# Kernel tuning notes

Measured on AMD Instinct MI355X. Metric: run time of the kernel, lower is better.

## Reference

```python
import jax, jax.numpy as jnp
import numpy as np

EPS = 1e-5
NEG_SLOPE = 0.01  # F.leaky_relu default

N0, N1, N2 = 100000, 25000, 5000
E0, E1 = 800000, 160000
D_IN, D_HID, D_OUT = 256, 256, 128


def setup_inputs() -> dict:
    key = jax.random.key(0)
    ks = jax.random.split(key, 16)
    inp = {
        "x": jax.random.normal(ks[0], (N0, D_IN), dtype=jnp.float32),
        "src0": jax.random.randint(ks[1], (E0,), 0, N0, dtype=jnp.int32),
        "dst0": jax.random.randint(ks[2], (E0,), 0, N1, dtype=jnp.int32),
        "val0": jnp.arange(E0, dtype=jnp.int32),
        "src1": jax.random.randint(ks[3], (E1,), 0, N1, dtype=jnp.int32),
        "dst1": jax.random.randint(ks[4], (E1,), 0, N2, dtype=jnp.int32),
        "val1": jnp.arange(E1, dtype=jnp.int32),
        "timestamps": jax.random.randint(ks[5], (E0 + E1,), 0, 100, dtype=jnp.int32),
        "time": 50,
        "interval": 10,
        # SAGEConv layer 1 (in -> hidden): lin_l (bias) on aggregated, lin_r (no bias) on root
        "W1l": jax.random.normal(ks[6], (D_IN, D_HID), dtype=jnp.float32) / np.sqrt(D_IN),
        "W1r": jax.random.normal(ks[7], (D_IN, D_HID), dtype=jnp.float32) / np.sqrt(D_IN),
        "b1": jnp.zeros((D_HID,), dtype=jnp.float32),
        # BatchNorm1d params (eval mode: running stats)
        "g1": jnp.ones((D_HID,), dtype=jnp.float32),
        "bt1": jnp.zeros((D_HID,), dtype=jnp.float32),
        "rm1": jax.random.normal(ks[8], (D_HID,), dtype=jnp.float32) * 0.1,
        "rv1": jax.random.uniform(ks[9], (D_HID,), dtype=jnp.float32) + 0.5,
        # SAGEConv layer 2 (hidden -> out)
        "W2l": jax.random.normal(ks[10], (D_HID, D_OUT), dtype=jnp.float32) / np.sqrt(D_HID),
        "W2r": jax.random.normal(ks[11], (D_HID, D_OUT), dtype=jnp.float32) / np.sqrt(D_HID),
        "b2": jnp.zeros((D_OUT,), dtype=jnp.float32),
    }
    return inp


def _time_mask(val, timestamps, time, interval):
    # time_sparse keeps edges whose timestamp is in {time, ..., time+interval-1}
    ts = timestamps[val]
    return (ts >= time) & (ts < time + interval)


def _sage_conv(x_src, x_tgt, src, dst, mask, Wl, Wr, b, n_tgt):
    m = mask.astype(x_src.dtype)
    msg = x_src[src] * m[:, None]               # [E, D] gather + mask
    agg = jax.ops.segment_sum(msg, dst, num_segments=n_tgt)
    deg = jax.ops.segment_sum(m, dst, num_segments=n_tgt)
    agg = agg / jnp.maximum(deg, 1.0)[:, None]  # mean aggregation
    return agg @ Wl + b + x_tgt @ Wr


def reference(x, src0, dst0, val0, src1, dst1, val1, timestamps, time, interval,
              W1l, W1r, b1, g1, bt1, rm1, rv1, W2l, W2r, b2):
    # layer 0: N0 -> N1
    mask0 = _time_mask(val0, timestamps, time, interval)
    h = _sage_conv(x, x[:N1], src0, dst0, mask0, W1l, W1r, b1, N1)
    # BatchNorm1d (eval) + leaky_relu; dropout is identity in eval
    h = (h - rm1) * jax.lax.rsqrt(rv1 + EPS) * g1 + bt1
    h = jnp.where(h >= 0, h, NEG_SLOPE * h)
    # layer 1: N1 -> N2
    mask1 = _time_mask(val1, timestamps, time, interval)
    out = _sage_conv(h, h[:N2], src1, dst1, mask1, W2l, W2r, b2, N2)
    return out, mask1
```

## Files before the change

kernel.cpp:

```cpp
#include <hip/hip_runtime.h>

#define N1c 25000
#define N2c 5000
#define Dc 256
#define DOUTc 128
#define EPSc 1e-5f
#define NEGc 0.01f
#define CAPc 32

typedef __attribute__((ext_vector_type(8))) short short8;
typedef __attribute__((ext_vector_type(4))) float f32x4;

__device__ __forceinline__ ushort f2bf(float f) {
    unsigned u = __float_as_uint(f);
    u += 0x7fffu + ((u >> 16) & 1u);
    return (ushort)(u >> 16);
}
__device__ __forceinline__ float bf2f(ushort u) {
    return __uint_as_float(((unsigned)u) << 16);
}

__global__ __launch_bounds__(256) void prep_fill(
    const int* __restrict__ src0, const int* __restrict__ dst0, const int* __restrict__ val0,
    const int* __restrict__ src1, const int* __restrict__ dst1, const int* __restrict__ val1,
    const int* __restrict__ ts, const int* __restrict__ time_p, const int* __restrict__ itv_p,
    const float* __restrict__ W1l, const float* __restrict__ W1r,
    const float* __restrict__ W2l, const float* __restrict__ W2r,
    int E0, int E1,
    ushort* __restrict__ Bt1, ushort* __restrict__ Bt2,
    int* __restrict__ cnt0, int* __restrict__ cnt1,
    int* __restrict__ eidx0, int* __restrict__ eidx1,
    float* __restrict__ mask_out) {
    const int flat = blockIdx.x * blockDim.x + threadIdx.x;
    const int NT = gridDim.x * blockDim.x;
    const int t0 = *time_p, iv = *itv_p;

    for (int i = flat; i < 256 * 512; i += NT) {
        int n = i >> 9, k = i & 511;
        float v = (k < 256) ? W1l[(size_t)k * 256 + n] : W1r[(size_t)(k - 256) * 256 + n];
        Bt1[i] = f2bf(v);
    }
    for (int i = flat; i < 128 * 512; i += NT) {
        int n = i >> 9, k = i & 511;
        float v = (k < 256) ? W2l[(size_t)k * 128 + n] : W2r[(size_t)(k - 256) * 128 + n];
        Bt2[i] = f2bf(v);
    }
    for (int e = flat; e < E0; e += NT) {
        int t = ts[val0[e]];
        if (t >= t0 && t < t0 + iv) {
            int d = dst0[e];
            int pos = atomicAdd(&cnt0[d], 1);
            if (pos < CAPc) eidx0[d * CAPc + pos] = src0[e];
        }
    }
    for (int e = flat; e < E1; e += NT) {
        int t = ts[val1[e]];
        bool m = (t >= t0 && t < t0 + iv);
        mask_out[e] = m ? 1.0f : 0.0f;
        if (m) {
            int d = dst1[e];
            int pos = atomicAdd(&cnt1[d], 1);
            if (pos < CAPc) eidx1[d * CAPc + pos] = src1[e];
        }
    }
}

template <int VARIANT, int BMT, int NJW>
__global__ __launch_bounds__(512) void fused_gemm(
    const void* __restrict__ Asrc,
    const int* __restrict__ cnt, const int* __restrict__ eidx,
    const int* __restrict__ src, const int* __restrict__ dst,
    const int* __restrict__ val, const int* __restrict__ ts,
    const int* __restrict__ time_p, const int* __restrict__ itv_p, int E,
    const ushort* __restrict__ Bt,
    const float* __restrict__ bias,
    const float* __restrict__ g, const float* __restrict__ bt,
    const float* __restrict__ rm, const float* __restrict__ rv,
    void* __restrict__ Cout, int M) {
    constexpr int RT = BMT / 16;
    constexpr int RPW = BMT / 8;
    __shared__ ushort As[BMT][536];
    const int tid = threadIdx.x;
    const int wave = tid >> 6, lane = tid & 63;
    const int quad = lane >> 4, l16 = lane & 15;
    const int m0 = blockIdx.x * BMT;
    const float* Xf = (const float*)Asrc;
    const ushort* Hb = (const ushort*)Asrc;

    for (int i = 0; i < RPW; ++i) {
        int r = wave * RPW + i;
        int m = m0 + r;
        if (m >= M) {
            *(ushort4*)&As[r][lane * 4] = make_ushort4(0, 0, 0, 0);
            *(ushort4*)&As[r][256 + lane * 4] = make_ushort4(0, 0, 0, 0);
            continue;
        }
        int c = cnt[m];
        int my = (lane < CAPc) ? eidx[m * CAPc + lane] : 0;
        float4 a0 = make_float4(0.f, 0.f, 0.f, 0.f);
        float4 a1 = make_float4(0.f, 0.f, 0.f, 0.f);
        if (c <= CAPc) {
            int j = 0;
            for (; j + 1 < c; j += 2) {
                int s0 = __shfl(my, j, 64);
                int s1 = __shfl(my, j + 1, 64);
                if (VARIANT == 0) {
                    float4 v0 = *(const float4*)(Xf + (size_t)s0 * Dc + lane * 4);
                    float4 v1 = *(const float4*)(Xf + (size_t)s1 * Dc + lane * 4);
                    a0.x += v0.x; a0.y += v0.y; a0.z += v0.z; a0.w += v0.w;
                    a1.x += v1.x; a1.y += v1.y; a1.z += v1.z; a1.w += v1.w;
                } else {
                    ushort4 v0 = *(const ushort4*)(Hb + (size_t)s0 * Dc + lane * 4);
                    ushort4 v1 = *(const ushort4*)(Hb + (size_t)s1 * Dc + lane * 4);
                    a0.x += bf2f(v0.x); a0.y += bf2f(v0.y); a0.z += bf2f(v0.z); a0.w += bf2f(v0.w);
                    a1.x += bf2f(v1.x); a1.y += bf2f(v1.y); a1.z += bf2f(v1.z); a1.w += bf2f(v1.w);
                }
            }
            if (j < c) {
                int s0 = __shfl(my, j, 64);
                if (VARIANT == 0) {
                    float4 v0 = *(const float4*)(Xf + (size_t)s0 * Dc + lane * 4);
                    a0.x += v0.x; a0.y += v0.y; a0.z += v0.z; a0.w += v0.w;
                } else {
                    ushort4 v0 = *(const ushort4*)(Hb + (size_t)s0 * Dc + lane * 4);
                    a0.x += bf2f(v0.x); a0.y += bf2f(v0.y); a0.z += bf2f(v0.z); a0.w += bf2f(v0.w);
                }
            }
        } else {
            int t0 = *time_p, iv = *itv_p;
            for (int e = 0; e < E; ++e) {
                if (dst[e] != m) continue;
                int t = ts[val[e]];
                if (t >= t0 && t < t0 + iv) {
                    if (VARIANT == 0) {
                        float4 v = *(const float4*)(Xf + (size_t)src[e] * Dc + lane * 4);
                        a0.x += v.x; a0.y += v.y; a0.z += v.z; a0.w += v.w;
                    } else {
                        ushort4 v = *(const ushort4*)(Hb + (size_t)src[e] * Dc + lane * 4);
                        a0.x += bf2f(v.x); a0.y += bf2f(v.y); a0.z += bf2f(v.z); a0.w += bf2f(v.w);
                    }
                }
            }
        }
        a0.x += a1.x; a0.y += a1.y; a0.z += a1.z; a0.w += a1.w;
        float inv = 1.0f / fmaxf((float)c, 1.0f);
        ushort4 o;
        o.x = f2bf(a0.x * inv); o.y = f2bf(a0.y * inv);
        o.z = f2bf(a0.z * inv); o.w = f2bf(a0.w * inv);
        *(ushort4*)&As[r][lane * 4] = o;
        if (VARIANT == 0) {
            float4 rt = *(const float4*)(Xf + (size_t)m * Dc + lane * 4);
            ushort4 ro;
            ro.x = f2bf(rt.x); ro.y = f2bf(rt.y); ro.z = f2bf(rt.z); ro.w = f2bf(rt.w);
            *(ushort4*)&As[r][256 + lane * 4] = ro;
        } else {
            *(ushort4*)&As[r][256 + lane * 4] = *(const ushort4*)(Hb + (size_t)m * Dc + lane * 4);
        }
    }
    __syncthreads();

    f32x4 acc[RT][NJW] = {};
    const ushort* Bw = Bt + (size_t)((wave * NJW) * 16 + l16) * 512 + quad * 8;
    for (int k0 = 0; k0 < 512; k0 += 32) {
        short8 af[RT];
#pragma unroll
        for (int rt = 0; rt < RT; ++rt)
            af[rt] = *(const short8*)&As[rt * 16 + l16][k0 + quad * 8];
        uint4 bfr[NJW];
#pragma unroll
        for (int jj = 0; jj < NJW; ++jj)
            bfr[jj] = *(const uint4*)(Bw + (size_t)jj * 16 * 512 + k0);
#pragma unroll
        for (int jj = 0; jj < NJW; ++jj) {
            short8 bf = *reinterpret_cast<const short8*>(&bfr[jj]);
#pragma unroll
            for (int rt = 0; rt < RT; ++rt)
                acc[rt][jj] = __builtin_amdgcn_mfma_f32_16x16x32_bf16(af[rt], bf, acc[rt][jj], 0, 0, 0);
        }
    }

#pragma unroll
    for (int jj = 0; jj < NJW; ++jj) {
        int gn = (wave * NJW + jj) * 16 + l16;
        float sc = 1.f, sh = bias[gn];
        if (VARIANT == 0) {
            float s = g[gn] * rsqrtf(rv[gn] + EPSc);
            sh = (bias[gn] - rm[gn]) * s + bt[gn];
            sc = s;
        }
#pragma unroll
        for (int rt = 0; rt < RT; ++rt) {
            int gmb = m0 + rt * 16 + quad * 4;
#pragma unroll
            for (int rr = 0; rr < 4; ++rr) {
                int gm = gmb + rr;
                if (gm >= M) continue;
                float v = acc[rt][jj][rr];
                if (VARIANT == 0) {
                    v = v * sc + sh;
                    v = v >= 0.f ? v : NEGc * v;
                    ((ushort*)Cout)[(size_t)gm * Dc + gn] = f2bf(v);
                } else {
                    ((float*)Cout)[(size_t)gm * DOUTc + gn] = v + sh;
                }
            }
        }
    }
}

extern "C" void kernel_launch(void* const* d_in, const int* in_sizes, int n_in,
                              void* d_out, int out_size, void* d_ws, size_t ws_size,
                              hipStream_t stream) {
    const float* x    = (const float*)d_in[0];
    const int* src0   = (const int*)d_in[1];
    const int* dst0   = (const int*)d_in[2];
    const int* val0   = (const int*)d_in[3];
    const int* src1   = (const int*)d_in[4];
    const int* dst1   = (const int*)d_in[5];
    const int* val1   = (const int*)d_in[6];
    const int* ts     = (const int*)d_in[7];
    const int* time_p = (const int*)d_in[8];
    const int* itv_p  = (const int*)d_in[9];
    const float* W1l  = (const float*)d_in[10];
    const float* W1r  = (const float*)d_in[11];
    const float* b1   = (const float*)d_in[12];
    const float* g1   = (const float*)d_in[13];
    const float* bt1  = (const float*)d_in[14];
    const float* rm1  = (const float*)d_in[15];
    const float* rv1  = (const float*)d_in[16];
    const float* W2l  = (const float*)d_in[17];
    const float* W2r  = (const float*)d_in[18];
    const float* b2   = (const float*)d_in[19];
    int E0 = in_sizes[1];
    int E1 = in_sizes[4];
    float* out = (float*)d_out;

    ushort* h    = (ushort*)d_ws;
    ushort* Bt1  = h    + (size_t)N1c * Dc;
    ushort* Bt2  = Bt1  + 256 * 512;
    int* ip      = (int*)(Bt2 + 128 * 512);
    int* cnt0    = ip;             ip += N1c;
    int* cnt1    = ip;             ip += N2c;
    int* eidx0   = ip;             ip += N1c * CAPc;
    int* eidx1   = ip;             ip += N2c * CAPc;
    float* mask_tail = out + (size_t)N2c * DOUTc;

    hipMemsetAsync(cnt0, 0, (size_t)(N1c + N2c) * sizeof(int), stream);

    prep_fill<<<2048, 256, 0, stream>>>(
        src0, dst0, val0, src1, dst1, val1, ts, time_p, itv_p,
        W1l, W1r, W2l, W2r, E0, E1, Bt1, Bt2,
        cnt0, cnt1, eidx0, eidx1, mask_tail);
    fused_gemm<0, 32, 2><<<(N1c + 31) / 32, 512, 0, stream>>>(
        x, cnt0, eidx0, src0, dst0, val0, ts, time_p, itv_p, E0,
        Bt1, b1, g1, bt1, rm1, rv1, h, N1c);
    fused_gemm<1, 16, 1><<<(N2c + 15) / 16, 512, 0, stream>>>(
        h, cnt1, eidx1, src1, dst1, val1, ts, time_p, itv_p, E1,
        Bt2, b2, nullptr, nullptr, nullptr, nullptr, out, N2c);
}
```

Before: 248.7 us.

## Batch gather loads across rows to raise memory-level parallelism in aggregation

```diff
diff --git a/kernel.cpp b/kernel.cpp
--- a/kernel.cpp
+++ b/kernel.cpp
@@ -19,6 +19,8 @@
 __device__ __forceinline__ float bf2f(ushort u) {
     return __uint_as_float(((unsigned)u) << 16);
 }
+__device__ __forceinline__ int imin(int a, int b) { return a < b ? a : b; }
+__device__ __forceinline__ int imax(int a, int b) { return a > b ? a : b; }
 
 __global__ __launch_bounds__(256) void prep_fill(
     const int* __restrict__ src0, const int* __restrict__ dst0, const int* __restrict__ val0,
@@ -87,74 +89,124 @@
     const float* Xf = (const float*)Asrc;
     const ushort* Hb = (const ushort*)Asrc;
 
+    int ms_[RPW], cs_[RPW], my_[RPW];
+#pragma unroll
     for (int i = 0; i < RPW; ++i) {
-        int r = wave * RPW + i;
-        int m = m0 + r;
-        if (m >= M) {
-            *(ushort4*)&As[r][lane * 4] = make_ushort4(0, 0, 0, 0);
-            *(ushort4*)&As[r][256 + lane * 4] = make_ushort4(0, 0, 0, 0);
-            continue;
-        }
-        int c = cnt[m];
-        int my = (lane < CAPc) ? eidx[m * CAPc + lane] : 0;
-        float4 a0 = make_float4(0.f, 0.f, 0.f, 0.f);
-        float4 a1 = make_float4(0.f, 0.f, 0.f, 0.f);
-        if (c <= CAPc) {
-            int j = 0;
-            for (; j + 1 < c; j += 2) {
-                int s0 = __shfl(my, j, 64);
-                int s1 = __shfl(my, j + 1, 64);
-                if (VARIANT == 0) {
-                    float4 v0 = *(const float4*)(Xf + (size_t)s0 * Dc + lane * 4);
-                    float4 v1 = *(const float4*)(Xf + (size_t)s1 * Dc + lane * 4);
-                    a0.x += v0.x; a0.y += v0.y; a0.z += v0.z; a0.w += v0.w;
-                    a1.x += v1.x; a1.y += v1.y; a1.z += v1.z; a1.w += v1.w;
-                } else {
-                    ushort4 v0 = *(const ushort4*)(Hb + (size_t)s0 * Dc + lane * 4);
-                    ushort4 v1 = *(const ushort4*)(Hb + (size_t)s1 * Dc + lane * 4);
-                    a0.x += bf2f(v0.x); a0.y += bf2f(v0.y); a0.z += bf2f(v0.z); a0.w += bf2f(v0.w);
-                    a1.x += bf2f(v1.x); a1.y += bf2f(v1.y); a1.z += bf2f(v1.z); a1.w += bf2f(v1.w);
+        ms_[i] = m0 + wave * RPW + i;
+        cs_[i] = (ms_[i] < M) ? cnt[ms_[i]] : 0;
+    }
+#pragma unroll
+    for (int i = 0; i < RPW; ++i)
+        my_[i] = (ms_[i] < M && lane < CAPc) ? eidx[ms_[i] * CAPc + lane] : 0;
+    float4 rtf_[RPW];
+    ushort4 rtb_[RPW];
+#pragma unroll
+    for (int i = 0; i < RPW; ++i) {
+        int mm = imax(0, imin(ms_[i], M - 1));
+        if (VARIANT == 0) rtf_[i] = *(const float4*)(Xf + (size_t)mm * Dc + lane * 4);
+        else              rtb_[i] = *(const ushort4*)(Hb + (size_t)mm * Dc + lane * 4);
+    }
+#pragma unroll
+    for (int i = 0; i < RPW; ++i)
+        my_[i] = (lane < cs_[i]) ? my_[i] : 0;
+
+    float4 acc_[RPW];
+#pragma unroll
+    for (int i = 0; i < RPW; ++i) acc_[i] = make_float4(0.f, 0.f, 0.f, 0.f);
+
+#pragma unroll
+    for (int p = 0; p < RPW; p += 2) {
+        float4 vf[2][4];
+        ushort4 vb[2][4];
+        int ccs[2];
+#pragma unroll
+        for (int q = 0; q < 2; ++q) {
+            int cc = imin(cs_[p + q], CAPc);
+            ccs[q] = cc;
+#pragma unroll
+            for (int u = 0; u < 4; ++u) {
+                int e = imax(0, imin(u, cc - 1));
+                int s = __shfl(my_[p + q], e, 64);
+                if (VARIANT == 0) vf[q][u] = *(const float4*)(Xf + (size_t)s * Dc + lane * 4);
+                else              vb[q][u] = *(const ushort4*)(Hb + (size_t)s * Dc + lane * 4);
+            }
+        }
+#pragma unroll
+        for (int q = 0; q < 2; ++q) {
+            int i = p + q;
+            int cc = ccs[q];
+#pragma unroll
+            for (int u = 0; u < 4; ++u) {
+                if (u < cc) {
+                    if (VARIANT == 0) {
+                        acc_[i].x += vf[q][u].x; acc_[i].y += vf[q][u].y;
+                        acc_[i].z += vf[q][u].z; acc_[i].w += vf[q][u].w;
+                    } else {
+                        acc_[i].x += bf2f(vb[q][u].x); acc_[i].y += bf2f(vb[q][u].y);
+                        acc_[i].z += bf2f(vb[q][u].z); acc_[i].w += bf2f(vb[q][u].w);
+                    }
                 }
             }
-            if (j < c) {
-                int s0 = __shfl(my, j, 64);
-                if (VARIANT == 0) {
-                    float4 v0 = *(const float4*)(Xf + (size_t)s0 * Dc + lane * 4);
-                    a0.x += v0.x; a0.y += v0.y; a0.z += v0.z; a0.w += v0.w;
-                } else {
-                    ushort4 v0 = *(const ushort4*)(Hb + (size_t)s0 * Dc + lane * 4);
-                    a0.x += bf2f(v0.x); a0.y += bf2f(v0.y); a0.z += bf2f(v0.z); a0.w += bf2f(v0.w);
+            for (int jb = 4; jb < cc; jb += 4) {
+#pragma unroll
+                for (int u = 0; u < 4; ++u) {
+                    int e = imin(jb + u, cc - 1);
+                    int s = __shfl(my_[i], e, 64);
+                    if (jb + u < cc) {
+                        if (VARIANT == 0) {
+                            float4 v = *(const float4*)(Xf + (size_t)s * Dc + lane * 4);
+                            acc_[i].x += v.x; acc_[i].y += v.y; acc_[i].z += v.z; acc_[i].w += v.w;
+                        } else {
+                            ushort4 v = *(const ushort4*)(Hb + (size_t)s * Dc + lane * 4);
+                            acc_[i].x += bf2f(v.x); acc_[i].y += bf2f(v.y);
+                            acc_[i].z += bf2f(v.z); acc_[i].w += bf2f(v.w);
+                        }
+                    }
                 }
             }
-        } else {
+        }
+    }
+#pragma unroll
+    for (int i = 0; i < RPW; ++i) {
+        if (cs_[i] > CAPc) {
+            float4 a = make_float4(0.f, 0.f, 0.f, 0.f);
             int t0 = *time_p, iv = *itv_p;
             for (int e = 0; e < E; ++e) {
-                if (dst[e] != m) continue;
+                if (dst[e] != ms_[i]) continue;
                 int t = ts[val[e]];
                 if (t >= t0 && t < t0 + iv) {
                     if (VARIANT == 0) {
                         float4 v = *(const float4*)(Xf + (size_t)src[e] * Dc + lane * 4);
-                        a0.x += v.x; a0.y += v.y; a0.z += v.z; a0.w += v.w;
+                        a.x += v.x; a.y += v.y; a.z += v.z; a.w += v.w;
                     } else {
                         ushort4 v = *(const ushort4*)(Hb + (size_t)src[e] * Dc + lane * 4);
-                        a0.x += bf2f(v.x); a0.y += bf2f(v.y); a0.z += bf2f(v.z); a0.w += bf2f(v.w);
+                        a.x += bf2f(v.x); a.y += bf2f(v.y); a.z += bf2f(v.z); a.w += bf2f(v.w);
                     }
                 }
             }
-        }
-        a0.x += a1.x; a0.y += a1.y; a0.z += a1.z; a0.w += a1.w;
-        float inv = 1.0f / fmaxf((float)c, 1.0f);
+            acc_[i] = a;
+        }
+    }
+#pragma unroll
+    for (int i = 0; i < RPW; ++i) {
+        int r = wave * RPW + i;
+        if (ms_[i] >= M) {
+            *(ushort4*)&As[r][lane * 4] = make_ushort4(0, 0, 0, 0);
+            *(ushort4*)&As[r][256 + lane * 4] = make_ushort4(0, 0, 0, 0);
+            continue;
+        }
+        float inv = 1.0f / fmaxf((float)cs_[i], 1.0f);
         ushort4 o;
-        o.x = f2bf(a0.x * inv); o.y = f2bf(a0.y * inv);
-        o.z = f2bf(a0.z * inv); o.w = f2bf(a0.w * inv);
+        o.x = f2bf(acc_[i].x * inv); o.y = f2bf(acc_[i].y * inv);
+        o.z = f2bf(acc_[i].z * inv); o.w = f2bf(acc_[i].w * inv);
         *(ushort4*)&As[r][lane * 4] = o;
         if (VARIANT == 0) {
-            float4 rt = *(const float4*)(Xf + (size_t)m * Dc + lane * 4);
             ushort4 ro;
-            ro.x = f2bf(rt.x); ro.y = f2bf(rt.y); ro.z = f2bf(rt.z); ro.w = f2bf(rt.w);
+            ro.x = f2bf(rtf_[i].x); ro.y = f2bf(rtf_[i].y);
+            ro.z = f2bf(rtf_[i].z); ro.w = f2bf(rtf_[i].w);
             *(ushort4*)&As[r][256 + lane * 4] = ro;
         } else {
-            *(ushort4*)&As[r][256 + lane * 4] = *(const ushort4*)(Hb + (size_t)m * Dc + lane * 4);
+            *(ushort4*)&As[r][256 + lane * 4] = rtb_[i];
         }
     }
     __syncthreads();
```

After: 248.9 us. No clear change (+0.1%).

## Fuse whole pipeline into one cooperative persistent kernel with grid syncs

Applied to the files above, without the earlier changes.

```diff
diff --git a/kernel.cpp b/kernel.cpp
--- a/kernel.cpp
+++ b/kernel.cpp
@@ -1,4 +1,7 @@
 #include <hip/hip_runtime.h>
+#include <hip/hip_cooperative_groups.h>
+
+namespace cg = cooperative_groups;
 
 #define N1c 25000
 #define N2c 5000
@@ -18,6 +21,250 @@
 }
 __device__ __forceinline__ float bf2f(ushort u) {
     return __uint_as_float(((unsigned)u) << 16);
+}
+__device__ __forceinline__ unsigned pack2(float lo, float hi) {
+    return ((unsigned)f2bf(lo)) | (((unsigned)f2bf(hi)) << 16);
+}
+
+struct MegaParams {
+    const float* x;
+    const int *src0, *dst0, *val0, *src1, *dst1, *val1, *ts, *time_p, *itv_p;
+    const float *W1l, *W1r, *b1, *g1, *bt1, *rm1, *rv1, *W2l, *W2r, *b2;
+    int E0, E1;
+    ushort *agg0, *h, *agg1, *Bt1, *Bt2;
+    int *cnt0, *cnt1, *eidx0, *eidx1;
+    float *mask_out, *out;
+};
+
+template <int SRC>
+__device__ __forceinline__ void gather_phase(
+    const void* Xsrc, const int* cnt, const int* eidx,
+    const int* src, const int* dst, const int* val, const int* ts,
+    int t0, int iv, int E, ushort* agg, int n, int gw, int nw, int lane) {
+    const float* Xf = (const float*)Xsrc;
+    const ushort* Hb = (const ushort*)Xsrc;
+    for (int row = gw; row < n; row += nw) {
+        int c = cnt[row];
+        int my = (lane < CAPc) ? eidx[row * CAPc + lane] : 0;
+        my = (lane < c) ? my : 0;
+        float4 a = make_float4(0.f, 0.f, 0.f, 0.f);
+        float4 a2 = make_float4(0.f, 0.f, 0.f, 0.f);
+        if (c <= CAPc) {
+            int j = 0;
+            for (; j + 1 < c; j += 2) {
+                int s0 = __shfl(my, j, 64);
+                int s1 = __shfl(my, j + 1, 64);
+                if (SRC == 0) {
+                    float4 v0 = *(const float4*)(Xf + (size_t)s0 * Dc + lane * 4);
+                    float4 v1 = *(const float4*)(Xf + (size_t)s1 * Dc + lane * 4);
+                    a.x += v0.x; a.y += v0.y; a.z += v0.z; a.w += v0.w;
+                    a2.x += v1.x; a2.y += v1.y; a2.z += v1.z; a2.w += v1.w;
+                } else {
+                    ushort4 v0 = *(const ushort4*)(Hb + (size_t)s0 * Dc + lane * 4);
+                    ushort4 v1 = *(const ushort4*)(Hb + (size_t)s1 * Dc + lane * 4);
+                    a.x += bf2f(v0.x); a.y += bf2f(v0.y);
+                    a.z += bf2f(v0.z); a.w += bf2f(v0.w);
+                    a2.x += bf2f(v1.x); a2.y += bf2f(v1.y);
+                    a2.z += bf2f(v1.z); a2.w += bf2f(v1.w);
+                }
+            }
+            if (j < c) {
+                int s0 = __shfl(my, j, 64);
+                if (SRC == 0) {
+                    float4 v0 = *(const float4*)(Xf + (size_t)s0 * Dc + lane * 4);
+                    a.x += v0.x; a.y += v0.y; a.z += v0.z; a.w += v0.w;
+                } else {
+                    ushort4 v0 = *(const ushort4*)(Hb + (size_t)s0 * Dc + lane * 4);
+                    a.x += bf2f(v0.x); a.y += bf2f(v0.y);
+                    a.z += bf2f(v0.z); a.w += bf2f(v0.w);
+                }
+            }
+        } else {
+            for (int e = 0; e < E; ++e) {
+                if (dst[e] != row) continue;
+                int t = ts[val[e]];
+                if (t >= t0 && t < t0 + iv) {
+                    if (SRC == 0) {
+                        float4 v = *(const float4*)(Xf + (size_t)src[e] * Dc + lane * 4);
+                        a.x += v.x; a.y += v.y; a.z += v.z; a.w += v.w;
+                    } else {
+                        ushort4 v = *(const ushort4*)(Hb + (size_t)src[e] * Dc + lane * 4);
+                        a.x += bf2f(v.x); a.y += bf2f(v.y);
+                        a.z += bf2f(v.z); a.w += bf2f(v.w);
+                    }
+                }
+            }
+        }
+        a.x += a2.x; a.y += a2.y; a.z += a2.z; a.w += a2.w;
+        float inv = 1.0f / fmaxf((float)c, 1.0f);
+        ushort4 o;
+        o.x = f2bf(a.x * inv); o.y = f2bf(a.y * inv);
+        o.z = f2bf(a.z * inv); o.w = f2bf(a.w * inv);
+        *(ushort4*)(agg + (size_t)row * Dc + lane * 4) = o;
+    }
+}
+
+template <int VARIANT>
+__device__ __forceinline__ void gemm_tile(
+    ushort (*As)[536], int mt,
+    const ushort* Alo, const void* A2, const ushort* Bt,
+    const float* bias, const float* g, const float* bt,
+    const float* rm, const float* rv, void* Cout, int M, int tid) {
+    constexpr int NJW = (VARIANT == 0) ? 4 : 2;
+    const int wave = tid >> 6, lane = tid & 63;
+    const int quad = lane >> 4, l16 = lane & 15;
+    const int m0 = mt * 32;
+#pragma unroll
+    for (int i = 0; i < 8; ++i) {
+        int r = wave * 8 + i, m = m0 + r;
+        if (m < M) {
+            *(ushort4*)&As[r][lane * 4] =
+                *(const ushort4*)(Alo + (size_t)m * Dc + lane * 4);
+            if (VARIANT == 0) {
+                float4 xf = *(const float4*)((const float*)A2 + (size_t)m * Dc + lane * 4);
+                ushort4 ro;
+                ro.x = f2bf(xf.x); ro.y = f2bf(xf.y);
+                ro.z = f2bf(xf.z); ro.w = f2bf(xf.w);
+                *(ushort4*)&As[r][256 + lane * 4] = ro;
+            } else {
+                *(ushort4*)&As[r][256 + lane * 4] =
+                    *(const ushort4*)((const ushort*)A2 + (size_t)m * Dc + lane * 4);
+            }
+        } else {
+            *(ushort4*)&As[r][lane * 4] = make_ushort4(0, 0, 0, 0);
+            *(ushort4*)&As[r][256 + lane * 4] = make_ushort4(0, 0, 0, 0);
+        }
+    }
+    __syncthreads();
+    f32x4 acc[2][NJW] = {};
+    const ushort* Bw = Bt + (size_t)((wave * NJW) * 16 + l16) * 512 + quad * 8;
+    for (int k0 = 0; k0 < 512; k0 += 32) {
+        short8 af[2];
+        af[0] = *(const short8*)&As[l16][k0 + quad * 8];
+        af[1] = *(const short8*)&As[16 + l16][k0 + quad * 8];
+        uint4 bfr[NJW];
+#pragma unroll
+        for (int jj = 0; jj < NJW; ++jj)
+            bfr[jj] = *(const uint4*)(Bw + (size_t)jj * 16 * 512 + k0);
+#pragma unroll
+        for (int jj = 0; jj < NJW; ++jj) {
+            short8 bf = *reinterpret_cast<const short8*>(&bfr[jj]);
+#pragma unroll
+            for (int rt = 0; rt < 2; ++rt)
+                acc[rt][jj] = __builtin_amdgcn_mfma_f32_16x16x32_bf16(af[rt], bf, acc[rt][jj], 0, 0, 0);
+        }
+    }
+    __syncthreads();
+#pragma unroll
+    for (int jj = 0; jj < NJW; ++jj) {
+        int gn = (wave * NJW + jj) * 16 + l16;
+        float sc = 1.f, sh = bias[gn];
+        if (VARIANT == 0) {
+            float s = g[gn] * rsqrtf(rv[gn] + EPSc);
+            sh = (bias[gn] - rm[gn]) * s + bt[gn];
+            sc = s;
+        }
+#pragma unroll
+        for (int rt = 0; rt < 2; ++rt) {
+            int gmb = m0 + rt * 16 + quad * 4;
+#pragma unroll
+            for (int rr = 0; rr < 4; ++rr) {
+                int gm = gmb + rr;
+                if (gm >= M) continue;
+                float v = acc[rt][jj][rr];
+                if (VARIANT == 0) {
+                    v = v * sc + sh;
+                    v = v >= 0.f ? v : NEGc * v;
+                    ((ushort*)Cout)[(size_t)gm * Dc + gn] = f2bf(v);
+                } else {
+                    ((float*)Cout)[(size_t)gm * DOUTc + gn] = v + sh;
+                }
+            }
+        }
+    }
+}
+
+__global__ __launch_bounds__(256, 4) void mega(MegaParams P) {
+    cg::grid_group grid = cg::this_grid();
+    __shared__ ushort As[32][536];
+    const int tid = threadIdx.x, bid = blockIdx.x, nb = gridDim.x;
+    const int flat = bid * 256 + tid, NT = nb * 256;
+    const int lane = tid & 63;
+    const int gw = flat >> 6, nw = NT >> 6;
+    const int t0 = *P.time_p, iv = *P.itv_p;
+
+    for (int i = flat; i < N1c + N2c; i += NT) {
+        if (i < N1c) P.cnt0[i] = 0; else P.cnt1[i - N1c] = 0;
+    }
+    {
+        float (*tl)[33] = (float (*)[33])As;
+        const int tx = tid & 31, ty = tid >> 5;
+        for (int t = bid; t < 192; t += nb) {
+            const bool L1 = t < 128;
+            const int tt = L1 ? t : t - 128;
+            const int ntn = L1 ? 8 : 4;
+            const int kt = tt / ntn, nt = tt % ntn;
+            const int k0 = kt * 32, n0 = nt * 32;
+            const float* Wl = L1 ? P.W1l : P.W2l;
+            const float* Wr = L1 ? P.W1r : P.W2r;
+            const int nst = L1 ? 256 : 128;
+            ushort* Bt = L1 ? P.Bt1 : P.Bt2;
+#pragma unroll
+            for (int rr = 0; rr < 4; ++rr) {
+                int r = ty * 4 + rr;
+                int k = k0 + r;
+                tl[r][tx] = (k < 256) ? Wl[(size_t)k * nst + n0 + tx]
+                                      : Wr[(size_t)(k - 256) * nst + n0 + tx];
+            }
+            __syncthreads();
+#pragma unroll
+            for (int rr = 0; rr < 4; ++rr) {
+                int r = ty * 4 + rr;
+                Bt[(size_t)(n0 + r) * 512 + k0 + tx] = f2bf(tl[tx][r]);
+            }
+            __syncthreads();
+        }
+    }
+    for (int e = flat; e < P.E1; e += NT) {
+        int t = P.ts[P.val1[e]];
+        P.mask_out[e] = (t >= t0 && t < t0 + iv) ? 1.0f : 0.0f;
+    }
+    grid.sync();
+
+    for (int e = flat; e < P.E0; e += NT) {
+        int t = P.ts[P.val0[e]];
+        if (t >= t0 && t < t0 + iv) {
+            int d = P.dst0[e];
+            int pos = atomicAdd(&P.cnt0[d], 1);
+            if (pos < CAPc) P.eidx0[d * CAPc + pos] = P.src0[e];
+        }
+    }
+    for (int e = flat; e < P.E1; e += NT) {
+        int t = P.ts[P.val1[e]];
+        if (t >= t0 && t < t0 + iv) {
+            int d = P.dst1[e];
+            int pos = atomicAdd(&P.cnt1[d], 1);
+            if (pos < CAPc) P.eidx1[d * CAPc + pos] = P.src1[e];
+        }
+    }
+    grid.sync();
+
+    gather_phase<0>(P.x, P.cnt0, P.eidx0, P.src0, P.dst0, P.val0, P.ts,
+                    t0, iv, P.E0, P.agg0, N1c, gw, nw, lane);
+    grid.sync();
+
+    for (int mt = bid; mt * 32 < N1c; mt += nb)
+        gemm_tile<0>(As, mt, P.agg0, P.x, P.Bt1, P.b1, P.g1, P.bt1, P.rm1, P.rv1,
+                     P.h, N1c, tid);
+    grid.sync();
+
+    gather_phase<1>(P.h, P.cnt1, P.eidx1, P.src1, P.dst1, P.val1, P.ts,
+                    t0, iv, P.E1, P.agg1, N2c, gw, nw, lane);
+    grid.sync();
+
+    for (int mt = bid; mt * 32 < N2c; mt += nb)
+        gemm_tile<1>(As, mt, P.agg1, P.h, P.Bt2, P.b2, nullptr, nullptr, nullptr,
+                     nullptr, P.out, N2c, tid);
 }
 
 __global__ __launch_bounds__(256) void prep_fill(
@@ -34,16 +281,32 @@
     const int flat = blockIdx.x * blockDim.x + threadIdx.x;
     const int NT = gridDim.x * blockDim.x;
     const int t0 = *time_p, iv = *itv_p;
-
-    for (int i = flat; i < 256 * 512; i += NT) {
-        int n = i >> 9, k = i & 511;
-        float v = (k < 256) ? W1l[(size_t)k * 256 + n] : W1r[(size_t)(k - 256) * 256 + n];
-        Bt1[i] = f2bf(v);
-    }
-    for (int i = flat; i < 128 * 512; i += NT) {
-        int n = i >> 9, k = i & 511;
-        float v = (k < 256) ? W2l[(size_t)k * 128 + n] : W2r[(size_t)(k - 256) * 128 + n];
-        Bt2[i] = f2bf(v);
+    __shared__ float tl[32][33];
+    const int tx = threadIdx.x & 31, ty = threadIdx.x >> 5;
+    for (int t = blockIdx.x; t < 192; t += gridDim.x) {
+        const bool L1 = t < 128;
+        const int tt = L1 ? t : t - 128;
+        const int ntn = L1 ? 8 : 4;
+        const int kt = tt / ntn, nt = tt % ntn;
+        const int k0 = kt * 32, n0 = nt * 32;
+        const float* Wl = L1 ? W1l : W2l;
+        const float* Wr = L1 ? W1r : W2r;
+        const int nst = L1 ? 256 : 128;
+        ushort* Bt = L1 ? Bt1 : Bt2;
+#pragma unroll
+        for (int rr = 0; rr < 4; ++rr) {
+            int r = ty * 4 + rr;
+            int k = k0 + r;
+            tl[r][tx] = (k < 256) ? Wl[(size_t)k * nst + n0 + tx]
+                                  : Wr[(size_t)(k - 256) * nst + n0 + tx];
+        }
+        __syncthreads();
+#pragma unroll
+        for (int rr = 0; rr < 4; ++rr) {
+            int r = ty * 4 + rr;
+            Bt[(size_t)(n0 + r) * 512 + k0 + tx] = f2bf(tl[tx][r]);
+        }
+        __syncthreads();
     }
     for (int e = flat; e < E0; e += NT) {
         int t = ts[val0[e]];
@@ -65,147 +328,30 @@
     }
 }
 
-template <int VARIANT, int BMT, int NJW>
-__global__ __launch_bounds__(512) void fused_gemm(
-    const void* __restrict__ Asrc,
-    const int* __restrict__ cnt, const int* __restrict__ eidx,
-    const int* __restrict__ src, const int* __restrict__ dst,
-    const int* __restrict__ val, const int* __restrict__ ts,
-    const int* __restrict__ time_p, const int* __restrict__ itv_p, int E,
-    const ushort* __restrict__ Bt,
-    const float* __restrict__ bias,
+template <int SRC>
+__global__ void gather_k(const void* X, const int* __restrict__ cnt,
+                         const int* __restrict__ eidx,
+                         const int* __restrict__ src, const int* __restrict__ dst,
+                         const int* __restrict__ val, const int* __restrict__ ts,
+                         const int* __restrict__ time_p, const int* __restrict__ itv_p,
+                         int E, ushort* __restrict__ agg, int n) {
+    int wave = (blockIdx.x * blockDim.x + threadIdx.x) >> 6;
+    int lane = threadIdx.x & 63;
+    if (wave >= n) return;
+    gather_phase<SRC>(X, cnt, eidx, src, dst, val, ts, *time_p, *itv_p, E,
+                      agg, n, wave, 1 << 30, lane);
+}
+
+template <int VARIANT>
+__global__ __launch_bounds__(256) void gemm_k(
+    const ushort* __restrict__ Alo, const void* __restrict__ A2,
+    const ushort* __restrict__ Bt, const float* __restrict__ bias,
     const float* __restrict__ g, const float* __restrict__ bt,
     const float* __restrict__ rm, const float* __restrict__ rv,
     void* __restrict__ Cout, int M) {
-    constexpr int RT = BMT / 16;
-    constexpr int RPW = BMT / 8;
-    __shared__ ushort As[BMT][536];
-    const int tid = threadIdx.x;
-    const int wave = tid >> 6, lane = tid & 63;
-    const int quad = lane >> 4, l16 = lane & 15;
-    const int m0 = blockIdx.x * BMT;
-    const float* Xf = (const float*)Asrc;
-    const ushort* Hb = (const ushort*)Asrc;
-
-    for (int i = 0; i < RPW; ++i) {
-        int r = wave * RPW + i;
-        int m = m0 + r;
-        if (m >= M) {
-            *(ushort4*)&As[r][lane * 4] = make_ushort4(0, 0, 0, 0);
-            *(ushort4*)&As[r][256 + lane * 4] = make_ushort4(0, 0, 0, 0);
-            continue;
-        }
-        int c = cnt[m];
-        int my = (lane < CAPc) ? eidx[m * CAPc + lane] : 0;
-        float4 a0 = make_float4(0.f, 0.f, 0.f, 0.f);
-        float4 a1 = make_float4(0.f, 0.f, 0.f, 0.f);
-        if (c <= CAPc) {
-            int j = 0;
-            for (; j + 1 < c; j += 2) {
-                int s0 = __shfl(my, j, 64);
-                int s1 = __shfl(my, j + 1, 64);
-                if (VARIANT == 0) {
-                    float4 v0 = *(const float4*)(Xf + (size_t)s0 * Dc + lane * 4);
-                    float4 v1 = *(const float4*)(Xf + (size_t)s1 * Dc + lane * 4);
-                    a0.x += v0.x; a0.y += v0.y; a0.z += v0.z; a0.w += v0.w;
-                    a1.x += v1.x; a1.y += v1.y; a1.z += v1.z; a1.w += v1.w;
-                } else {
-                    ushort4 v0 = *(const ushort4*)(Hb + (size_t)s0 * Dc + lane * 4);
-                    ushort4 v1 = *(const ushort4*)(Hb + (size_t)s1 * Dc + lane * 4);
-                    a0.x += bf2f(v0.x); a0.y += bf2f(v0.y); a0.z += bf2f(v0.z); a0.w += bf2f(v0.w);
-                    a1.x += bf2f(v1.x); a1.y += bf2f(v1.y); a1.z += bf2f(v1.z); a1.w += bf2f(v1.w);
-                }
-            }
-            if (j < c) {
-                int s0 = __shfl(my, j, 64);
-                if (VARIANT == 0) {
-                    float4 v0 = *(const float4*)(Xf + (size_t)s0 * Dc + lane * 4);
-                    a0.x += v0.x; a0.y += v0.y; a0.z += v0.z; a0.w += v0.w;
-                } else {
-                    ushort4 v0 = *(const ushort4*)(Hb + (size_t)s0 * Dc + lane * 4);
-                    a0.x += bf2f(v0.x); a0.y += bf2f(v0.y); a0.z += bf2f(v0.z); a0.w += bf2f(v0.w);
-                }
-            }
-        } else {
-            int t0 = *time_p, iv = *itv_p;
-            for (int e = 0; e < E; ++e) {
-                if (dst[e] != m) continue;
-                int t = ts[val[e]];
-                if (t >= t0 && t < t0 + iv) {
-                    if (VARIANT == 0) {
-                        float4 v = *(const float4*)(Xf + (size_t)src[e] * Dc + lane * 4);
-                        a0.x += v.x; a0.y += v.y; a0.z += v.z; a0.w += v.w;
-                    } else {
-                        ushort4 v = *(const ushort4*)(Hb + (size_t)src[e] * Dc + lane * 4);
-                        a0.x += bf2f(v.x); a0.y += bf2f(v.y); a0.z += bf2f(v.z); a0.w += bf2f(v.w);
-                    }
-                }
-            }
-        }
-        a0.x += a1.x; a0.y += a1.y; a0.z += a1.z; a0.w += a1.w;
-        float inv = 1.0f / fmaxf((float)c, 1.0f);
-        ushort4 o;
-        o.x = f2bf(a0.x * inv); o.y = f2bf(a0.y * inv);
-        o.z = f2bf(a0.z * inv); o.w = f2bf(a0.w * inv);
-        *(ushort4*)&As[r][lane * 4] = o;
-        if (VARIANT == 0) {
-            float4 rt = *(const float4*)(Xf + (size_t)m * Dc + lane * 4);
-            ushort4 ro;
-            ro.x = f2bf(rt.x); ro.y = f2bf(rt.y); ro.z = f2bf(rt.z); ro.w = f2bf(rt.w);
-            *(ushort4*)&As[r][256 + lane * 4] = ro;
-        } else {
-            *(ushort4*)&As[r][256 + lane * 4] = *(const ushort4*)(Hb + (size_t)m * Dc + lane * 4);
-        }
-    }
-    __syncthreads();
-
-    f32x4 acc[RT][NJW] = {};
-    const ushort* Bw = Bt + (size_t)((wave * NJW) * 16 + l16) * 512 + quad * 8;
-    for (int k0 = 0; k0 < 512; k0 += 32) {
-        short8 af[RT];
-#pragma unroll
-        for (int rt = 0; rt < RT; ++rt)
-            af[rt] = *(const short8*)&As[rt * 16 + l16][k0 + quad * 8];
-        uint4 bfr[NJW];
-#pragma unroll
-        for (int jj = 0; jj < NJW; ++jj)
-            bfr[jj] = *(const uint4*)(Bw + (size_t)jj * 16 * 512 + k0);
-#pragma unroll
-        for (int jj = 0; jj < NJW; ++jj) {
-            short8 bf = *reinterpret_cast<const short8*>(&bfr[jj]);
-#pragma unroll
-            for (int rt = 0; rt < RT; ++rt)
-                acc[rt][jj] = __builtin_amdgcn_mfma_f32_16x16x32_bf16(af[rt], bf, acc[rt][jj], 0, 0, 0);
-        }
-    }
-
-#pragma unroll
-    for (int jj = 0; jj < NJW; ++jj) {
-        int gn = (wave * NJW + jj) * 16 + l16;
-        float sc = 1.f, sh = bias[gn];
-        if (VARIANT == 0) {
-            float s = g[gn] * rsqrtf(rv[gn] + EPSc);
-            sh = (bias[gn] - rm[gn]) * s + bt[gn];
-            sc = s;
-        }
-#pragma unroll
-        for (int rt = 0; rt < RT; ++rt) {
-            int gmb = m0 + rt * 16 + quad * 4;
-#pragma unroll
-            for (int rr = 0; rr < 4; ++rr) {
-                int gm = gmb + rr;
-                if (gm >= M) continue;
-                float v = acc[rt][jj][rr];
-                if (VARIANT == 0) {
-                    v = v * sc + sh;
-                    v = v >= 0.f ? v : NEGc * v;
-                    ((ushort*)Cout)[(size_t)gm * Dc + gn] = f2bf(v);
-                } else {
-                    ((float*)Cout)[(size_t)gm * DOUTc + gn] = v + sh;
-                }
-            }
-        }
-    }
+    __shared__ ushort As[32][536];
+    gemm_tile<VARIANT>(As, blockIdx.x, Alo, A2, Bt, bias, g, bt, rm, rv, Cout, M,
+                       threadIdx.x);
 }
 
 extern "C" void kernel_launch(void* const* d_in, const int* in_sizes, int n_in,
@@ -235,8 +381,10 @@
     int E1 = in_sizes[4];
     float* out = (float*)d_out;
 
-    ushort* h    = (ushort*)d_ws;
-    ushort* Bt1  = h    + (size_t)N1c * Dc;
+    ushort* agg0 = (ushort*)d_ws;
+    ushort* h    = agg0 + (size_t)N1c * Dc;
+    ushort* agg1 = h    + (size_t)N1c * Dc;
+    ushort* Bt1  = agg1 + (size_t)N2c * Dc;
     ushort* Bt2  = Bt1  + 256 * 512;
     int* ip      = (int*)(Bt2 + 128 * 512);
     int* cnt0    = ip;             ip += N1c;
@@ -245,16 +393,34 @@
     int* eidx1   = ip;             ip += N2c * CAPc;
     float* mask_tail = out + (size_t)N2c * DOUTc;
 
-    hipMemsetAsync(cnt0, 0, (size_t)(N1c + N2c) * sizeof(int), stream);
-
-    prep_fill<<<2048, 256, 0, stream>>>(
-        src0, dst0, val0, src1, dst1, val1, ts, time_p, itv_p,
-        W1l, W1r, W2l, W2r, E0, E1, Bt1, Bt2,
-        cnt0, cnt1, eidx0, eidx1, mask_tail);
-    fused_gemm<0, 32, 2><<<(N1c + 31) / 32, 512, 0, stream>>>(
-        x, cnt0, eidx0, src0, dst0, val0, ts, time_p, itv_p, E0,
-        Bt1, b1, g1, bt1, rm1, rv1, h, N1c);
-    fused_gemm<1, 16, 1><<<(N2c + 15) / 16, 512, 0, stream>>>(
-        h, cnt1, eidx1, src1, dst1, val1, ts, time_p, itv_p, E1,
-        Bt2, b2, nullptr, nullptr, nullptr, nullptr, out, N2c);
-}
+    MegaParams P;
+    P.x = x; P.src0 = src0; P.dst0 = dst0; P.val0 = val0;
+    P.src1 = src1; P.dst1 = dst1; P.val1 = val1;
+    P.ts = ts; P.time_p = time_p; P.itv_p = itv_p;
+    P.W1l = W1l; P.W1r = W1r; P.b1 = b1; P.g1 = g1; P.bt1 = bt1;
+    P.rm1 = rm1; P.rv1 = rv1; P.W2l = W2l; P.W2r = W2r; P.b2 = b2;
+    P.E0 = E0; P.E1 = E1;
+    P.agg0 = agg0; P.h = h; P.agg1 = agg1; P.Bt1 = Bt1; P.Bt2 = Bt2;
+    P.cnt0 = cnt0; P.cnt1 = cnt1; P.eidx0 = eidx0; P.eidx1 = eidx1;
+    P.mask_out = mask_tail; P.out = out;
+
+    void* args[] = {&P};
+    hipError_t err = hipLaunchCooperativeKernel(
+        (const void*)mega, dim3(1024), dim3(256), args, 0, stream);
+
+    if (err != hipSuccess) {
+        hipMemsetAsync(cnt0, 0, (size_t)(N1c + N2c) * sizeof(int), stream);
+        prep_fill<<<2048, 256, 0, stream>>>(
+            src0, dst0, val0, src1, dst1, val1, ts, time_p, itv_p,
+            W1l, W1r, W2l, W2r, E0, E1, Bt1, Bt2,
+            cnt0, cnt1, eidx0, eidx1, mask_tail);
+        gather_k<0><<<(N1c + 3) / 4, 256, 0, stream>>>(
+            x, cnt0, eidx0, src0, dst0, val0, ts, time_p, itv_p, E0, agg0, N1c);
+        gemm_k<0><<<(N1c + 31) / 32, 256, 0, stream>>>(
+            agg0, x, Bt1, b1, g1, bt1, rm1, rv1, h, N1c);
+        gather_k<1><<<(N2c + 3) / 4, 256, 0, stream>>>(
+            h, cnt1, eidx1, src1, dst1, val1, ts, time_p, itv_p, E1, agg1, N2c);
+        gemm_k<1><<<(N2c + 31) / 32, 256, 0, stream>>>(
+            agg1, h, Bt2, b2, nullptr, nullptr, nullptr, nullptr, out, N2c);
+    }
+}
```

Result: slower. 880.0 us (+253.9%).
